# Kernel tuning notes

Measured on AMD Instinct MI355X. Metric: run time of the kernel, lower is better.

## Reference

```python
import jax, jax.numpy as jnp
import numpy as np

K = 8              # kernel_size
C_IN = 3           # input_channels
HID = 256          # hidden_state_size
MID = 256          # mid_layer_size
N_MAIN = 4         # num_main_layers
N_CLS = 1000       # num_classes
N_PIX = K * K      # num_pixel_values
IN_VEC = 2 + 1 + N_PIX * C_IN + HID   # 451
OUT_VEC = 2 + 1 + HID                 # 259
B, H, W = 128, 256, 256


def _lin_init(k, fan_in, fan_out):
    kw, kb = jax.random.split(k)
    bound = 1.0 / np.sqrt(fan_in)
    w = jax.random.uniform(kw, (fan_in, fan_out), jnp.float32, -bound, bound)
    b = jax.random.uniform(kb, (fan_out,), jnp.float32, -bound, bound)
    return w, b


def setup_inputs() -> dict:
    key = jax.random.key(0)
    ks = jax.random.split(key, 16)
    image = jax.random.normal(ks[0], (B, C_IN, H, W), jnp.float32)
    locations = jax.random.uniform(ks[1], (B, 2), jnp.float32)
    scales = jax.random.uniform(ks[2], (B, 1), jnp.float32)
    hidden_state = jax.random.normal(ks[3], (B, HID), jnp.float32)
    w0, b0 = _lin_init(ks[4], IN_VEC, MID)
    rws, rbs = [], []
    for i in range(N_MAIN):
        w, b = _lin_init(jax.random.fold_in(ks[5], i), MID, MID)
        rws.append(w); rbs.append(b)
    rw = jnp.stack(rws); rb = jnp.stack(rbs)          # [4,MID,MID], [4,MID]
    wf, bf = _lin_init(ks[6], MID, OUT_VEC)
    cw0, cb0 = _lin_init(ks[7], HID, MID)
    crw, crb = _lin_init(ks[8], MID, MID)
    cw1, cb1 = _lin_init(ks[9], MID, N_CLS)
    return {"image": image, "locations": locations, "scales": scales,
            "hidden_state": hidden_state, "w0": w0, "b0": b0, "rw": rw,
            "rb": rb, "wf": wf, "bf": bf, "cw0": cw0, "cb0": cb0,
            "crw": crw, "crb": crb, "cw1": cw1, "cb1": cb1}


def fourier_interp_2d(image, sample_points):
    """Band-limited (NUDFT) interpolation of image at continuous points.
    image: [B,C,H,W]; sample_points: [B,N,2] in normalized [0,1) (ij order).
    Returns [B,N,C]."""
    Bsz, C, Hh, Ww = image.shape
    F = jnp.fft.fft2(image)                       # [B,C,H,W] complex
    fy = jnp.fft.fftfreq(Hh) * Hh                 # integer freqs [H]
    fx = jnp.fft.fftfreq(Ww) * Ww                 # integer freqs [W]
    y = sample_points[..., 0]                     # [B,N]
    x = sample_points[..., 1]
    two_pi_i = 2j * jnp.pi
    Ey = jnp.exp(two_pi_i * y[..., None] * fy)    # [B,N,H]
    Ex = jnp.exp(two_pi_i * x[..., None] * fx)    # [B,N,W]
    tmp = jnp.einsum('bchw,bnh->bcnw', F, Ey)     # dominant compute
    vals = jnp.einsum('bcnw,bnw->bcn', tmp, Ex).real / (Hh * Ww)
    return jnp.transpose(vals, (0, 2, 1))         # [B,N,C]


def reference(image, locations, scales, hidden_state,
              w0, b0, rw, rb, wf, bf, cw0, cb0, crw, crb, cw1, cb1):
    Bsz = image.shape[0]
    # base meshgrid: [K,K,2], ij indexing, values arange(K)/K
    g = jnp.arange(K, dtype=image.dtype) / K
    mesh = jnp.stack(jnp.meshgrid(g, g, indexing='ij'), axis=-1)  # [K,K,2]
    coords = mesh[None] - locations[:, None, None, :]             # [B,K,K,2]
    coords = coords * scales[:, None, None, :]
    coords = coords.reshape(Bsz, N_PIX, 2)
    pix = fourier_interp_2d(image, coords)                        # [B,N,C]
    pix = pix.reshape(Bsz, N_PIX * C_IN)
    inp = jnp.concatenate([locations, scales, pix, hidden_state], axis=-1)
    h = inp @ w0 + b0
    for i in range(N_MAIN):
        h = jax.nn.relu(h @ rw[i] + rb[i] + h)
    out = jnp.tanh(h @ wf + bf)                                   # [B,OUT_VEC]
    new_loc = locations + out[:, :2]
    new_scale = scales + out[:, 2:3]
    new_hidden = hidden_state + out[:, 3:]
    c = jax.nn.relu(new_hidden @ cw0 + cb0)
    c = jax.nn.relu(c @ crw + crb + c)
    preds = jax.nn.softmax(c @ cw1 + cb1, axis=-1)
    # concat all outputs: [B, 2+1+HID+N_CLS]
    return jnp.concatenate([new_loc, new_scale, new_hidden, preds], axis=-1)
```

## Files before the change

kernel.cpp:

```cpp
#include <hip/hip_runtime.h>
#include <math.h>

#define BB 128
#define OUTROW 1259

typedef float vf4 __attribute__((ext_vector_type(4)));

__device__ __forceinline__ ushort f2b(float x) {
    unsigned u = __float_as_uint(x);
    unsigned r = (u + 0x7FFFu + ((u >> 16) & 1u)) >> 16;
    return (ushort)r;
}
__device__ __forceinline__ uint pack2(float lo, float hi) {
    return (uint)f2b(lo) | ((uint)f2b(hi) << 16);
}
__device__ __forceinline__ float dot2bf(uint a, uint b, float c) {
    float d;
    asm("v_dot2_f32_bf16 %0, %1, %2, %3" : "=v"(d) : "v"(a), "v"(b), "v"(c));
    return d;
}

#define OFF_W0   0u
#define OFF_RW   122880u
#define OFF_CW0  385024u
#define OFF_CRW  450560u
#define OFF_WF   516096u
#define OFF_CW1  582656u
#define N_TOT    838656u

__device__ __forceinline__ void dirichlet_ab(float t, float& A, float& Bv) {
    float r = t - rintf(t);
    float s256 = sinpif(256.0f * r);
    Bv = s256 * (1.0f / 256.0f);
    if (fabsf(r) < 1e-6f) {
        A = 1.0f;
    } else {
        float sp = sinpif(r), cp = cospif(r);
        A = Bv * cp / sp;
    }
}

__global__ __launch_bounds__(256) void interp_convert_kernel(
    const float* __restrict__ image, const float* __restrict__ loc,
    const float* __restrict__ scl, float* __restrict__ pix,
    const float* __restrict__ w0, const float* __restrict__ rw,
    const float* __restrict__ wf, const float* __restrict__ cw0,
    const float* __restrict__ crw, const float* __restrict__ cw1,
    ushort* __restrict__ bfa)
{
    __shared__ float U[256 * 16];
    __shared__ float V[16 * 260];
    __shared__ float T[16 * 260];

    int bid = blockIdx.x;
    int tid = threadIdx.x;

    if (bid >= 384) {
        unsigned g = (unsigned)(bid - 384) * 256u + (unsigned)tid;
        for (unsigned j = g; j < N_TOT; j += 512u * 256u) {
            ushort v;
            if (j < 122880u) {
                unsigned kp = j >> 9, r = j & 511u, c = r >> 1, k = 2u*kp + (r & 1u);
                v = (k < 451u) ? f2b(w0[k * 256u + c]) : (ushort)0;
            } else if (j < 385024u) {
                unsigned jj = j - 122880u;
                unsigned kp = jj >> 9, r = jj & 511u, c = r >> 1, k = 2u*kp + (r & 1u);
                v = f2b(rw[k * 256u + c]);
            } else if (j < 450560u) {
                unsigned jj = j - 385024u;
                unsigned kp = jj >> 9, r = jj & 511u, c = r >> 1, k = 2u*kp + (r & 1u);
                v = f2b(cw0[k * 256u + c]);
            } else if (j < 516096u) {
                unsigned jj = j - 450560u;
                unsigned kp = jj >> 9, r = jj & 511u, c = r >> 1, k = 2u*kp + (r & 1u);
                v = f2b(crw[k * 256u + c]);
            } else if (j < 582656u) {
                unsigned jj = j - 516096u;
                unsigned kp = jj / 520u, r = jj - kp * 520u, c = r >> 1, k = 2u*kp + (r & 1u);
                v = (c < 259u) ? f2b(wf[k * 259u + c]) : (ushort)0;
            } else {
                unsigned jj = j - 582656u;
                unsigned kp = jj / 2000u, r = jj - kp * 2000u, c = r >> 1, k = 2u*kp + (r & 1u);
                v = f2b(cw1[k * 1000u + c]);
            }
            __builtin_nontemporal_store(v, &bfa[j]);
        }
        return;
    }

    int b = bid / 3, c = bid % 3;
    float l0 = loc[2 * b], l1 = loc[2 * b + 1], sc = scl[b];

    {
        int p = tid;
        float tp = (float)p * (1.0f / 256.0f);
        #pragma unroll
        for (int iy = 0; iy < 8; ++iy) {
            float A, Bv;
            float y = ((float)iy * 0.125f - l0) * sc;
            dirichlet_ab(y - tp, A, Bv);
            int w = iy >> 1, o = iy & 1;
            U[p * 16 + w * 4 + o] = A;
            U[p * 16 + w * 4 + 2 + o] = Bv;
            float x = ((float)iy * 0.125f - l1) * sc;
            dirichlet_ab(x - tp, A, Bv);
            V[iy * 260 + p] = A;
            V[(8 + iy) * 260 + p] = Bv;
        }
    }
    __syncthreads();

    int wave = tid >> 6, lane = tid & 63;
    const float* img = image + (size_t)(b * 3 + c) * 65536 + lane * 4;

    float aA0[4] = {0, 0, 0, 0}, aA1[4] = {0, 0, 0, 0};
    float aB0[4] = {0, 0, 0, 0}, aB1[4] = {0, 0, 0, 0};
    #pragma unroll 4
    for (int p = 0; p < 256; ++p) {
        vf4 v = __builtin_nontemporal_load((const vf4*)(img + p * 256));
        const float4 u = *(const float4*)(&U[p * 16 + wave * 4]);
        aA0[0] += u.x * v[0]; aA0[1] += u.x * v[1]; aA0[2] += u.x * v[2]; aA0[3] += u.x * v[3];
        aA1[0] += u.y * v[0]; aA1[1] += u.y * v[1]; aA1[2] += u.y * v[2]; aA1[3] += u.y * v[3];
        aB0[0] += u.z * v[0]; aB0[1] += u.z * v[1]; aB0[2] += u.z * v[2]; aB0[3] += u.z * v[3];
        aB1[0] += u.w * v[0]; aB1[1] += u.w * v[1]; aB1[2] += u.w * v[2]; aB1[3] += u.w * v[3];
    }
    int iy0 = wave * 2;
    int q0 = lane * 4;
    #pragma unroll
    for (int j = 0; j < 4; ++j) {
        T[iy0 * 260 + q0 + j]       = aA0[j];
        T[(iy0 + 1) * 260 + q0 + j] = aA1[j];
        T[(8 + iy0) * 260 + q0 + j]     = aB0[j];
        T[(8 + iy0 + 1) * 260 + q0 + j] = aB1[j];
    }
    __syncthreads();

    int n = tid >> 2, sub = tid & 3;
    int iy = n >> 3, ix = n & 7;
    float s = 0.f;
    #pragma unroll 8
    for (int i = 0; i < 64; ++i) {
        int q = sub + 4 * i;
        s += T[iy * 260 + q] * V[ix * 260 + q] - T[(8 + iy) * 260 + q] * V[(8 + ix) * 260 + q];
    }
    s += __shfl_xor(s, 1);
    s += __shfl_xor(s, 2);
    if (sub == 0) pix[(b * 64 + n) * 3 + c] = s;
}

__global__ __launch_bounds__(1024, 1) void mlp_fused(
    const float* __restrict__ loc, const float* __restrict__ scl,
    const float* __restrict__ hidden, const float* __restrict__ pix,
    const ushort* __restrict__ bfa,
    const float* __restrict__ b0, const float* __restrict__ rb,
    const float* __restrict__ bf, const float* __restrict__ cb0,
    const float* __restrict__ crb, const float* __restrict__ cb1,
    float* __restrict__ out, float* __restrict__ sink)
{
    __shared__ float s_in[480];
    __shared__ float s_h[256];
    __shared__ float s_c[256];
    __shared__ float s_o[260];
    __shared__ float s_part[16 * 260];
    __shared__ float s_lg[1024];
    __shared__ uint  s_in2[240];
    __shared__ uint  s_hb2[128];
    __shared__ uint  s_cb2[128];
    __shared__ float s_b0[256], s_rb[1024], s_bf[260], s_cb0[256], s_crb[256], s_cb1[1000];
    __shared__ float s_red[32];

    int bid = blockIdx.x, tid = threadIdx.x;

    if (bid >= BB) {
        const uint* A = (const uint*)bfa;
        int w = bid - BB;
        int slice = w >> 3;
        unsigned SL = 26208u;
        unsigned lo = slice * SL, hi = lo + SL;
        float acc = 0.f;
        for (int it = 0; it < 16; ++it) {
            for (unsigned i = lo + tid * 4u; i + 3u < hi; i += 4096u) {
                uint4 v = *(const uint4*)(A + i);
                acc += (float)(v.x ^ v.y ^ v.z ^ v.w);
            }
        }
        if (acc == 1.0e30f) sink[0] = acc;
        return;
    }

    int b = bid;
    int jg = tid & 63, sub = tid >> 6;
    int j4 = jg * 4;
    float* orow = out + (size_t)b * OUTROW;

    if (tid < 2) s_in[tid] = loc[2 * b + tid];
    if (tid == 2) s_in[2] = scl[b];
    if (tid >= 256 && tid < 448) s_in[3 + (tid - 256)] = pix[b * 192 + (tid - 256)];
    if (tid >= 512 && tid < 768) s_in[195 + (tid - 512)] = hidden[b * 256 + (tid - 512)];
    if (tid >= 768 && tid < 797) s_in[451 + (tid - 768)] = 0.f;
    if (tid < 256) s_b0[tid] = b0[tid];
    s_rb[tid] = rb[tid];
    if (tid < 259) s_bf[tid] = bf[tid];
    if (tid >= 256 && tid < 512) s_cb0[tid - 256] = cb0[tid - 256];
    if (tid >= 512 && tid < 768) s_crb[tid - 512] = crb[tid - 512];
    if (tid < 1000) s_cb1[tid] = cb1[tid];
    __syncthreads();
    if (tid < 240) s_in2[tid] = pack2(s_in[2 * tid], s_in[2 * tid + 1]);
    __syncthreads();

    const ushort* w0b  = bfa + OFF_W0;
    const ushort* rwb  = bfa + OFF_RW;
    const ushort* cw0b = bfa + OFF_CW0;
    const ushort* crwb = bfa + OFF_CRW;
    const ushort* wfb  = bfa + OFF_WF;
    const ushort* cw1b = bfa + OFF_CW1;

    {
        uint4 wv[15]; uint hv[15];
        #pragma unroll
        for (int t = 0; t < 15; ++t)
            wv[t] = *(const uint4*)(w0b + (size_t)(sub + 16 * t) * 512 + jg * 8);
        #pragma unroll
        for (int t = 0; t < 15; ++t) hv[t] = s_in2[sub + 16 * t];
        vf4 a = {0.f, 0.f, 0.f, 0.f};
        #pragma unroll
        for (int t = 0; t < 15; ++t) {
            a[0] = dot2bf(wv[t].x, hv[t], a[0]);
            a[1] = dot2bf(wv[t].y, hv[t], a[1]);
            a[2] = dot2bf(wv[t].z, hv[t], a[2]);
            a[3] = dot2bf(wv[t].w, hv[t], a[3]);
        }
        *(vf4*)(&s_part[sub * 256 + j4]) = a;
    }
    __syncthreads();
    if (tid < 256) {
        float v = s_b0[tid];
        #pragma unroll
        for (int s = 0; s < 16; ++s) v += s_part[s * 256 + tid];
        s_h[tid] = v;
        float v2 = __shfl_xor(v, 1);
        if (!(tid & 1)) s_hb2[tid >> 1] = pack2(v, v2);
    }
    __syncthreads();

    #pragma unroll 1
    for (int L = 0; L < 4; ++L) {
        const ushort* W = rwb + (size_t)L * 65536;
        {
            uint4 wv[8]; uint hv[8];
            #pragma unroll
            for (int t = 0; t < 8; ++t)
                wv[t] = *(const uint4*)(W + (size_t)(sub + 16 * t) * 512 + jg * 8);
            #pragma unroll
            for (int t = 0; t < 8; ++t) hv[t] = s_hb2[sub + 16 * t];
            vf4 a = {0.f, 0.f, 0.f, 0.f};
            #pragma unroll
            for (int t = 0; t < 8; ++t) {
                a[0] = dot2bf(wv[t].x, hv[t], a[0]);
                a[1] = dot2bf(wv[t].y, hv[t], a[1]);
                a[2] = dot2bf(wv[t].z, hv[t], a[2]);
                a[3] = dot2bf(wv[t].w, hv[t], a[3]);
            }
            *(vf4*)(&s_part[sub * 256 + j4]) = a;
        }
        __syncthreads();
        if (tid < 256) {
            float v = s_rb[L * 256 + tid] + s_h[tid];
            #pragma unroll
            for (int s = 0; s < 16; ++s) v += s_part[s * 256 + tid];
            v = fmaxf(v, 0.f);
            s_h[tid] = v;
            float v2 = __shfl_xor(v, 1);
            if (!(tid & 1)) s_hb2[tid >> 1] = pack2(v, v2);
        }
        __syncthreads();
    }

    {
        uint4 wv[8]; uint hv[8];
        #pragma unroll
        for (int t = 0; t < 8; ++t)
            wv[t] = *(const uint4*)(wfb + (size_t)(sub + 16 * t) * 520 + jg * 8);
        #pragma unroll
        for (int t = 0; t < 8; ++t) hv[t] = s_hb2[sub + 16 * t];
        vf4 a = {0.f, 0.f, 0.f, 0.f};
        #pragma unroll
        for (int t = 0; t < 8; ++t) {
            a[0] = dot2bf(wv[t].x, hv[t], a[0]);
            a[1] = dot2bf(wv[t].y, hv[t], a[1]);
            a[2] = dot2bf(wv[t].z, hv[t], a[2]);
            a[3] = dot2bf(wv[t].w, hv[t], a[3]);
        }
        *(vf4*)(&s_part[sub * 260 + j4]) = a;
        if (jg < 4) {
            float e = 0.f;
            #pragma unroll
            for (int t = 0; t < 8; ++t) {
                uint w = *(const uint*)(wfb + (size_t)(sub + 16 * t) * 520 + 512 + jg * 2);
                e = dot2bf(w, hv[t], e);
            }
            s_part[sub * 260 + 256 + jg] = e;
        }
    }
    __syncthreads();
    if (tid < 259) {
        float v = s_bf[tid];
        #pragma unroll
        for (int s = 0; s < 16; ++s) v += s_part[s * 260 + tid];
        s_o[tid] = tanhf(v);
    }
    __syncthreads();

    if (tid < 256) {
        float nh = s_in[195 + tid] + s_o[3 + tid];
        orow[3 + tid] = nh;
        s_h[tid] = nh;
        float v2 = __shfl_xor(nh, 1);
        if (!(tid & 1)) s_hb2[tid >> 1] = pack2(nh, v2);
    }
    if (tid == 256) orow[0] = s_in[0] + s_o[0];
    if (tid == 257) orow[1] = s_in[1] + s_o[1];
    if (tid == 258) orow[2] = s_in[2] + s_o[2];
    __syncthreads();

    {
        uint4 wv[8]; uint hv[8];
        #pragma unroll
        for (int t = 0; t < 8; ++t)
            wv[t] = *(const uint4*)(cw0b + (size_t)(sub + 16 * t) * 512 + jg * 8);
        #pragma unroll
        for (int t = 0; t < 8; ++t) hv[t] = s_hb2[sub + 16 * t];
        vf4 a = {0.f, 0.f, 0.f, 0.f};
        #pragma unroll
        for (int t = 0; t < 8; ++t) {
            a[0] = dot2bf(wv[t].x, hv[t], a[0]);
            a[1] = dot2bf(wv[t].y, hv[t], a[1]);
            a[2] = dot2bf(wv[t].z, hv[t], a[2]);
            a[3] = dot2bf(wv[t].w, hv[t], a[3]);
        }
        *(vf4*)(&s_part[sub * 256 + j4]) = a;
    }
    __syncthreads();
    if (tid < 256) {
        float v = s_cb0[tid];
        #pragma unroll
        for (int s = 0; s < 16; ++s) v += s_part[s * 256 + tid];
        v = fmaxf(v, 0.f);
        s_c[tid] = v;
        float v2 = __shfl_xor(v, 1);
        if (!(tid & 1)) s_cb2[tid >> 1] = pack2(v, v2);
    }
    __syncthreads();

    {
        uint4 wv[8]; uint hv[8];
        #pragma unroll
        for (int t = 0; t < 8; ++t)
            wv[t] = *(const uint4*)(crwb + (size_t)(sub + 16 * t) * 512 + jg * 8);
        #pragma unroll
        for (int t = 0; t < 8; ++t) hv[t] = s_cb2[sub + 16 * t];
        vf4 a = {0.f, 0.f, 0.f, 0.f};
        #pragma unroll
        for (int t = 0; t < 8; ++t) {
            a[0] = dot2bf(wv[t].x, hv[t], a[0]);
            a[1] = dot2bf(wv[t].y, hv[t], a[1]);
            a[2] = dot2bf(wv[t].z, hv[t], a[2]);
            a[3] = dot2bf(wv[t].w, hv[t], a[3]);
        }
        *(vf4*)(&s_part[sub * 256 + j4]) = a;
    }
    __syncthreads();
    if (tid < 256) {
        float v = s_crb[tid] + s_c[tid];
        #pragma unroll
        for (int s = 0; s < 16; ++s) v += s_part[s * 256 + tid];
        v = fmaxf(v, 0.f);
        float v2 = __shfl_xor(v, 1);
        if (!(tid & 1)) s_cb2[tid >> 1] = pack2(v, v2);
    }
    __syncthreads();

    int jg8 = tid & 127, sub8 = tid >> 7;
    int c4 = jg8 * 4;
    {
        uint4 wv[16]; uint hv[16];
        #pragma unroll
        for (int t = 0; t < 16; ++t)
            wv[t] = *(const uint4*)(cw1b + (size_t)(sub8 + 8 * t) * 2000 + c4 * 2);
        #pragma unroll
        for (int t = 0; t < 16; ++t) hv[t] = s_cb2[sub8 + 8 * t];
        vf4 a = {0.f, 0.f, 0.f, 0.f};
        #pragma unroll
        for (int t = 0; t < 16; ++t) {
            a[0] = dot2bf(wv[t].x, hv[t], a[0]);
            a[1] = dot2bf(wv[t].y, hv[t], a[1]);
            a[2] = dot2bf(wv[t].z, hv[t], a[2]);
            a[3] = dot2bf(wv[t].w, hv[t], a[3]);
        }
        *(vf4*)(&s_part[sub8 * 512 + c4]) = a;
    }
    __syncthreads();
    if (tid < 512) {
        float v = s_cb1[tid];
        #pragma unroll
        for (int s = 0; s < 8; ++s) v += s_part[s * 512 + tid];
        s_lg[tid] = v;
    }
    __syncthreads();

    {
        vf4 a = {0.f, 0.f, 0.f, 0.f};
        if (jg8 < 122) {
            uint4 wv[16]; uint hv[16];
            #pragma unroll
            for (int t = 0; t < 16; ++t)
                wv[t] = *(const uint4*)(cw1b + (size_t)(sub8 + 8 * t) * 2000 + (512 + c4) * 2);
            #pragma unroll
            for (int t = 0; t < 16; ++t) hv[t] = s_cb2[sub8 + 8 * t];
            #pragma unroll
            for (int t = 0; t < 16; ++t) {
                a[0] = dot2bf(wv[t].x, hv[t], a[0]);
                a[1] = dot2bf(wv[t].y, hv[t], a[1]);
                a[2] = dot2bf(wv[t].z, hv[t], a[2]);
                a[3] = dot2bf(wv[t].w, hv[t], a[3]);
            }
        }
        *(vf4*)(&s_part[sub8 * 512 + c4]) = a;
    }
    __syncthreads();
    if (tid < 488) {
        float v = s_cb1[512 + tid];
        #pragma unroll
        for (int s = 0; s < 8; ++s) v += s_part[s * 512 + tid];
        s_lg[512 + tid] = v;
    }
    __syncthreads();

    float lgv = (tid < 1000) ? s_lg[tid] : -1e30f;
    int lane = tid & 63, wid = tid >> 6;
    float m = lgv;
    #pragma unroll
    for (int off = 1; off < 64; off <<= 1) m = fmaxf(m, __shfl_xor(m, off));
    if (lane == 0) s_red[wid] = m;
    __syncthreads();
    m = s_red[0];
    #pragma unroll
    for (int w = 1; w < 16; ++w) m = fmaxf(m, s_red[w]);

    float e = (tid < 1000) ? expf(lgv - m) : 0.f;
    float lsum = e;
    #pragma unroll
    for (int off = 1; off < 64; off <<= 1) lsum += __shfl_xor(lsum, off);
    if (lane == 0) s_red[16 + wid] = lsum;
    __syncthreads();
    float total = 0.f;
    #pragma unroll
    for (int w = 0; w < 16; ++w) total += s_red[16 + w];

    if (tid < 1000) orow[259 + tid] = e / total;
}

extern "C" void kernel_launch(void* const* d_in, const int* in_sizes, int n_in,
                              void* d_out, int out_size, void* d_ws, size_t ws_size,
                              hipStream_t stream) {
    const float* image  = (const float*)d_in[0];
    const float* loc    = (const float*)d_in[1];
    const float* scl    = (const float*)d_in[2];
    const float* hidden = (const float*)d_in[3];
    const float* w0  = (const float*)d_in[4];
    const float* b0  = (const float*)d_in[5];
    const float* rw  = (const float*)d_in[6];
    const float* rb  = (const float*)d_in[7];
    const float* wf  = (const float*)d_in[8];
    const float* bf  = (const float*)d_in[9];
    const float* cw0 = (const float*)d_in[10];
    const float* cb0 = (const float*)d_in[11];
    const float* crw = (const float*)d_in[12];
    const float* crb = (const float*)d_in[13];
    const float* cw1 = (const float*)d_in[14];
    const float* cb1 = (const float*)d_in[15];

    float* ws   = (float*)d_ws;
    float* pix  = ws;
    ushort* bfa = (ushort*)(ws + 24576);
    float* sink = ws + 24576 + 419328 + 8;

    hipLaunchKernelGGL(interp_convert_kernel, dim3(384 + 512), dim3(256), 0, stream,
                       image, loc, scl, pix, w0, rw, wf, cw0, crw, cw1, bfa);
    hipLaunchKernelGGL(mlp_fused, dim3(256), dim3(1024), 0, stream,
                       loc, scl, hidden, pix, bfa,
                       b0, rb, bf, cb0, crb, cb1, (float*)d_out, sink);
}
```

Measured before the change: 71.67 us.

## Prefetch next layer's bf16 weights into registers across MLP layers

Replaces the per-layer load-then-compute pattern with a double-buffered register scheme. Two sets of eight uint4 registers (A and P) alternate, so each layer's weight tile is issued from global memory before the current layer's dot products and reductions run. This is meant to hide global load latency behind compute and barriers in the latency-bound per-sample MLP chain. It raises register pressure, which could lower occupancy or cause spills. The first layer is split into 8+7 chunks to keep the live register count down.

After: 71.48 us. About the same (-0.3%).

```diff
diff --git a/kernel.cpp b/kernel.cpp
--- a/kernel.cpp
+++ b/kernel.cpp
@@ -27,6 +27,34 @@
 #define OFF_WF   516096u
 #define OFF_CW1  582656u
 #define N_TOT    838656u
+
+#define LOADW8(V, BASE, STR) do { \
+    V##0 = *(const uint4*)((BASE) + (size_t)(sub +   0) * (STR) + jg * 8); \
+    V##1 = *(const uint4*)((BASE) + (size_t)(sub +  16) * (STR) + jg * 8); \
+    V##2 = *(const uint4*)((BASE) + (size_t)(sub +  32) * (STR) + jg * 8); \
+    V##3 = *(const uint4*)((BASE) + (size_t)(sub +  48) * (STR) + jg * 8); \
+    V##4 = *(const uint4*)((BASE) + (size_t)(sub +  64) * (STR) + jg * 8); \
+    V##5 = *(const uint4*)((BASE) + (size_t)(sub +  80) * (STR) + jg * 8); \
+    V##6 = *(const uint4*)((BASE) + (size_t)(sub +  96) * (STR) + jg * 8); \
+    V##7 = *(const uint4*)((BASE) + (size_t)(sub + 112) * (STR) + jg * 8); \
+} while (0)
+
+#define DOT1(V, H) do { \
+    a[0] = dot2bf(V.x, H, a[0]); a[1] = dot2bf(V.y, H, a[1]); \
+    a[2] = dot2bf(V.z, H, a[2]); a[3] = dot2bf(V.w, H, a[3]); \
+} while (0)
+
+#define DOT8(V, SRC) do { \
+    uint h_; \
+    h_ = (SRC)[sub +   0]; DOT1(V##0, h_); \
+    h_ = (SRC)[sub +  16]; DOT1(V##1, h_); \
+    h_ = (SRC)[sub +  32]; DOT1(V##2, h_); \
+    h_ = (SRC)[sub +  48]; DOT1(V##3, h_); \
+    h_ = (SRC)[sub +  64]; DOT1(V##4, h_); \
+    h_ = (SRC)[sub +  80]; DOT1(V##5, h_); \
+    h_ = (SRC)[sub +  96]; DOT1(V##6, h_); \
+    h_ = (SRC)[sub + 112]; DOT1(V##7, h_); \
+} while (0)
 
 __device__ __forceinline__ void dirichlet_ab(float t, float& A, float& Bv) {
     float r = t - rintf(t);
@@ -193,6 +221,9 @@
     int j4 = jg * 4;
     float* orow = out + (size_t)b * OUTROW;
 
+    uint4 A0, A1, A2, A3, A4, A5, A6, A7;
+    uint4 P0, P1, P2, P3, P4, P5, P6, P7;
+
     if (tid < 2) s_in[tid] = loc[2 * b + tid];
     if (tid == 2) s_in[2] = scl[b];
     if (tid >= 256 && tid < 448) s_in[3 + (tid - 256)] = pix[b * 192 + (tid - 256)];
@@ -216,44 +247,14 @@
     const ushort* cw1b = bfa + OFF_CW1;
 
     {
-        uint4 wv[15]; uint hv[15];
-        #pragma unroll
-        for (int t = 0; t < 15; ++t)
-            wv[t] = *(const uint4*)(w0b + (size_t)(sub + 16 * t) * 512 + jg * 8);
-        #pragma unroll
-        for (int t = 0; t < 15; ++t) hv[t] = s_in2[sub + 16 * t];
-        vf4 a = {0.f, 0.f, 0.f, 0.f};
-        #pragma unroll
-        for (int t = 0; t < 15; ++t) {
-            a[0] = dot2bf(wv[t].x, hv[t], a[0]);
-            a[1] = dot2bf(wv[t].y, hv[t], a[1]);
-            a[2] = dot2bf(wv[t].z, hv[t], a[2]);
-            a[3] = dot2bf(wv[t].w, hv[t], a[3]);
-        }
-        *(vf4*)(&s_part[sub * 256 + j4]) = a;
-    }
-    __syncthreads();
-    if (tid < 256) {
-        float v = s_b0[tid];
-        #pragma unroll
-        for (int s = 0; s < 16; ++s) v += s_part[s * 256 + tid];
-        s_h[tid] = v;
-        float v2 = __shfl_xor(v, 1);
-        if (!(tid & 1)) s_hb2[tid >> 1] = pack2(v, v2);
-    }
-    __syncthreads();
-
-    #pragma unroll 1
-    for (int L = 0; L < 4; ++L) {
-        const ushort* W = rwb + (size_t)L * 65536;
+        vf4 a = {0.f, 0.f, 0.f, 0.f};
         {
             uint4 wv[8]; uint hv[8];
             #pragma unroll
             for (int t = 0; t < 8; ++t)
-                wv[t] = *(const uint4*)(W + (size_t)(sub + 16 * t) * 512 + jg * 8);
-            #pragma unroll
-            for (int t = 0; t < 8; ++t) hv[t] = s_hb2[sub + 16 * t];
-            vf4 a = {0.f, 0.f, 0.f, 0.f};
+                wv[t] = *(const uint4*)(w0b + (size_t)(sub + 16 * t) * 512 + jg * 8);
+            #pragma unroll
+            for (int t = 0; t < 8; ++t) hv[t] = s_in2[sub + 16 * t];
             #pragma unroll
             for (int t = 0; t < 8; ++t) {
                 a[0] = dot2bf(wv[t].x, hv[t], a[0]);
@@ -261,43 +262,119 @@
                 a[2] = dot2bf(wv[t].z, hv[t], a[2]);
                 a[3] = dot2bf(wv[t].w, hv[t], a[3]);
             }
-            *(vf4*)(&s_part[sub * 256 + j4]) = a;
-        }
-        __syncthreads();
-        if (tid < 256) {
-            float v = s_rb[L * 256 + tid] + s_h[tid];
-            #pragma unroll
-            for (int s = 0; s < 16; ++s) v += s_part[s * 256 + tid];
-            v = fmaxf(v, 0.f);
-            s_h[tid] = v;
-            float v2 = __shfl_xor(v, 1);
-            if (!(tid & 1)) s_hb2[tid >> 1] = pack2(v, v2);
-        }
-        __syncthreads();
-    }
-
-    {
-        uint4 wv[8]; uint hv[8];
-        #pragma unroll
-        for (int t = 0; t < 8; ++t)
-            wv[t] = *(const uint4*)(wfb + (size_t)(sub + 16 * t) * 520 + jg * 8);
-        #pragma unroll
-        for (int t = 0; t < 8; ++t) hv[t] = s_hb2[sub + 16 * t];
-        vf4 a = {0.f, 0.f, 0.f, 0.f};
-        #pragma unroll
-        for (int t = 0; t < 8; ++t) {
-            a[0] = dot2bf(wv[t].x, hv[t], a[0]);
-            a[1] = dot2bf(wv[t].y, hv[t], a[1]);
-            a[2] = dot2bf(wv[t].z, hv[t], a[2]);
-            a[3] = dot2bf(wv[t].w, hv[t], a[3]);
-        }
+        }
+        {
+            uint4 wv[7]; uint hv[7];
+            #pragma unroll
+            for (int t = 0; t < 7; ++t)
+                wv[t] = *(const uint4*)(w0b + (size_t)(sub + 16 * (t + 8)) * 512 + jg * 8);
+            #pragma unroll
+            for (int t = 0; t < 7; ++t) hv[t] = s_in2[sub + 16 * (t + 8)];
+            #pragma unroll
+            for (int t = 0; t < 7; ++t) {
+                a[0] = dot2bf(wv[t].x, hv[t], a[0]);
+                a[1] = dot2bf(wv[t].y, hv[t], a[1]);
+                a[2] = dot2bf(wv[t].z, hv[t], a[2]);
+                a[3] = dot2bf(wv[t].w, hv[t], a[3]);
+            }
+        }
+        LOADW8(A, rwb, 512);
+        *(vf4*)(&s_part[sub * 256 + j4]) = a;
+    }
+    __syncthreads();
+    if (tid < 256) {
+        float v = s_b0[tid];
+        #pragma unroll
+        for (int s = 0; s < 16; ++s) v += s_part[s * 256 + tid];
+        s_h[tid] = v;
+        float v2 = __shfl_xor(v, 1);
+        if (!(tid & 1)) s_hb2[tid >> 1] = pack2(v, v2);
+    }
+    __syncthreads();
+
+    {
+        LOADW8(P, rwb + 65536, 512);
+        vf4 a = {0.f, 0.f, 0.f, 0.f};
+        DOT8(A, s_hb2);
+        *(vf4*)(&s_part[sub * 256 + j4]) = a;
+    }
+    __syncthreads();
+    if (tid < 256) {
+        float v = s_rb[tid] + s_h[tid];
+        #pragma unroll
+        for (int s = 0; s < 16; ++s) v += s_part[s * 256 + tid];
+        v = fmaxf(v, 0.f);
+        s_h[tid] = v;
+        float v2 = __shfl_xor(v, 1);
+        if (!(tid & 1)) s_hb2[tid >> 1] = pack2(v, v2);
+    }
+    __syncthreads();
+
+    {
+        LOADW8(A, rwb + 131072, 512);
+        vf4 a = {0.f, 0.f, 0.f, 0.f};
+        DOT8(P, s_hb2);
+        *(vf4*)(&s_part[sub * 256 + j4]) = a;
+    }
+    __syncthreads();
+    if (tid < 256) {
+        float v = s_rb[256 + tid] + s_h[tid];
+        #pragma unroll
+        for (int s = 0; s < 16; ++s) v += s_part[s * 256 + tid];
+        v = fmaxf(v, 0.f);
+        s_h[tid] = v;
+        float v2 = __shfl_xor(v, 1);
+        if (!(tid & 1)) s_hb2[tid >> 1] = pack2(v, v2);
+    }
+    __syncthreads();
+
+    {
+        LOADW8(P, rwb + 196608, 512);
+        vf4 a = {0.f, 0.f, 0.f, 0.f};
+        DOT8(A, s_hb2);
+        *(vf4*)(&s_part[sub * 256 + j4]) = a;
+    }
+    __syncthreads();
+    if (tid < 256) {
+        float v = s_rb[512 + tid] + s_h[tid];
+        #pragma unroll
+        for (int s = 0; s < 16; ++s) v += s_part[s * 256 + tid];
+        v = fmaxf(v, 0.f);
+        s_h[tid] = v;
+        float v2 = __shfl_xor(v, 1);
+        if (!(tid & 1)) s_hb2[tid >> 1] = pack2(v, v2);
+    }
+    __syncthreads();
+
+    {
+        LOADW8(A, wfb, 520);
+        vf4 a = {0.f, 0.f, 0.f, 0.f};
+        DOT8(P, s_hb2);
+        *(vf4*)(&s_part[sub * 256 + j4]) = a;
+    }
+    __syncthreads();
+    if (tid < 256) {
+        float v = s_rb[768 + tid] + s_h[tid];
+        #pragma unroll
+        for (int s = 0; s < 16; ++s) v += s_part[s * 256 + tid];
+        v = fmaxf(v, 0.f);
+        s_h[tid] = v;
+        float v2 = __shfl_xor(v, 1);
+        if (!(tid & 1)) s_hb2[tid >> 1] = pack2(v, v2);
+    }
+    __syncthreads();
+
+    {
+        LOADW8(P, cw0b, 512);
+        vf4 a = {0.f, 0.f, 0.f, 0.f};
+        DOT8(A, s_hb2);
         *(vf4*)(&s_part[sub * 260 + j4]) = a;
         if (jg < 4) {
             float e = 0.f;
             #pragma unroll
             for (int t = 0; t < 8; ++t) {
                 uint w = *(const uint*)(wfb + (size_t)(sub + 16 * t) * 520 + 512 + jg * 2);
-                e = dot2bf(w, hv[t], e);
+                e = dot2bf(w, s_hb2[sub + 16 * t], e);
             }
             s_part[sub * 260 + 256 + jg] = e;
         }
@@ -324,20 +401,9 @@
     __syncthreads();
 
     {
-        uint4 wv[8]; uint hv[8];
-        #pragma unroll
-        for (int t = 0; t < 8; ++t)
-            wv[t] = *(const uint4*)(cw0b + (size_t)(sub + 16 * t) * 512 + jg * 8);
-        #pragma unroll
-        for (int t = 0; t < 8; ++t) hv[t] = s_hb2[sub + 16 * t];
-        vf4 a = {0.f, 0.f, 0.f, 0.f};
-        #pragma unroll
-        for (int t = 0; t < 8; ++t) {
-            a[0] = dot2bf(wv[t].x, hv[t], a[0]);
-            a[1] = dot2bf(wv[t].y, hv[t], a[1]);
-            a[2] = dot2bf(wv[t].z, hv[t], a[2]);
-            a[3] = dot2bf(wv[t].w, hv[t], a[3]);
-        }
+        LOADW8(A, crwb, 512);
+        vf4 a = {0.f, 0.f, 0.f, 0.f};
+        DOT8(P, s_hb2);
         *(vf4*)(&s_part[sub * 256 + j4]) = a;
     }
     __syncthreads();
@@ -353,20 +419,8 @@
     __syncthreads();
 
     {
-        uint4 wv[8]; uint hv[8];
-        #pragma unroll
-        for (int t = 0; t < 8; ++t)
-            wv[t] = *(const uint4*)(crwb + (size_t)(sub + 16 * t) * 512 + jg * 8);
-        #pragma unroll
-        for (int t = 0; t < 8; ++t) hv[t] = s_cb2[sub + 16 * t];
-        vf4 a = {0.f, 0.f, 0.f, 0.f};
-        #pragma unroll
-        for (int t = 0; t < 8; ++t) {
-            a[0] = dot2bf(wv[t].x, hv[t], a[0]);
-            a[1] = dot2bf(wv[t].y, hv[t], a[1]);
-            a[2] = dot2bf(wv[t].z, hv[t], a[2]);
-            a[3] = dot2bf(wv[t].w, hv[t], a[3]);
-        }
+        vf4 a = {0.f, 0.f, 0.f, 0.f};
+        DOT8(A, s_cb2);
         *(vf4*)(&s_part[sub * 256 + j4]) = a;
     }
     __syncthreads();
```
